# Kernel tuning notes

Hardware: AMD Instinct MI355X
Metric: run time of the kernel (lower is better)

Reference implementation:

```python
import jax, jax.numpy as jnp
import numpy as np

EPS = 1e-5
PROJ_EPS = 1e-5
MAX_TANH_ARG = 15.0
NUM_LAYERS = 2

def _norm(x):
    return jnp.sqrt(jnp.sum(x * x, axis=-1, keepdims=True))

def log_map_zero(y):
    # Poincare ball log map at the origin: arctanh(||y||) * y / ||y||
    n = _norm(y)
    n_c = jnp.clip(n, EPS, 1.0 - PROJ_EPS)
    return jnp.arctanh(n_c) * y / jnp.maximum(n, EPS)

def exp_map_zero(v):
    # Poincare ball exp map at the origin: tanh(||v||) * v / ||v||
    n = _norm(v)
    n_c = jnp.clip(n, EPS, MAX_TANH_ARG)
    return jnp.tanh(n_c) * v / jnp.maximum(n, EPS)

def setup_inputs() -> dict:
    key = jax.random.key(0)
    k1, k2, k3, k4 = jax.random.split(key, 4)
    N, K, D = 50000, 32, 128
    # scale initial features so they lie inside the unit ball
    node_repr = jax.random.normal(k1, (N, D), dtype=jnp.float32) * 0.01
    adj_mat = jax.random.randint(k2, (N, K), 0, N, dtype=jnp.int32)
    weight = jax.random.uniform(k3, (N, K), dtype=jnp.float32)
    mask = jnp.ones((N, 1), dtype=jnp.float32)
    # learned params: one [D, D] matrix per layer (tie_weight=False, poincare)
    msg_weights = jax.random.normal(k4, (NUM_LAYERS, D, D), dtype=jnp.float32) * (1.0 / np.sqrt(D))
    return {"node_repr": node_repr, "adj_mat": adj_mat, "weight": weight,
            "mask": mask, "msg_weights": msg_weights}

def reference(node_repr, adj_mat, weight, mask, msg_weights):
    x = node_repr
    for step in range(NUM_LAYERS):
        # log map back to tangent space at origin (identity on first layer)
        x = (log_map_zero(x) if step > 0 else x) * mask
        msg = (x @ msg_weights[step]) * mask            # [N, D] dense projection
        nbr = msg[adj_mat]                              # [N, K, D] gather by adjacency
        combined = jnp.einsum('nk,nkd->nd', weight, nbr) * mask  # weighted neighbor sum (dropout p=0)
        x = exp_map_zero(combined) * mask               # back to the manifold
        x = jax.nn.relu(x) * mask                       # poincare activation
    return x
```

## Files before the change

### kernel.cpp

```cpp
#include <hip/hip_runtime.h>

#define EPS 1e-5f
#define PROJ_EPS 1e-5f
#define MAX_TANH_ARG 15.0f

typedef __bf16 bf16x8 __attribute__((ext_vector_type(8)));
typedef float f32x4 __attribute__((ext_vector_type(4)));

__device__ __forceinline__ unsigned short f2bf(float f) {
  unsigned u = __builtin_bit_cast(unsigned, f);
  u += 0x7fffu + ((u >> 16) & 1u);
  return (unsigned short)(u >> 16);
}
__device__ __forceinline__ float bf2f(unsigned short h) {
  return __builtin_bit_cast(float, ((unsigned)h) << 16);
}

union BF8 {
  unsigned short u[8];
  bf16x8 v;
  uint4 q;
};

__global__ void pack_w_kernel(const float* __restrict__ W,
                              unsigned short* __restrict__ wpack) {
  int tid = blockIdx.x * blockDim.x + threadIdx.x;
  if (tid >= 2 * 8 * 4 * 64) return;
  int lane = tid & 63;
  int s = (tid >> 6) & 3;
  int t = (tid >> 8) & 7;
  int layer = tid >> 11;
  int quad = lane >> 4;
  int n = t * 16 + (lane & 15);
  unsigned short* dst = wpack + ((size_t)((layer * 32 + t * 4 + s) * 64 + lane)) * 8;
  const float* src = W + (size_t)layer * 16384;
#pragma unroll
  for (int j = 0; j < 8; ++j) {
    int k = s * 32 + quad * 8 + j;
    dst[j] = f2bf(src[(size_t)k * 128 + n]);
  }
}

template <int MODE>
__global__ __launch_bounds__(256) void gemm_kernel(
    const float* __restrict__ xf, const unsigned short* __restrict__ xb,
    const float* __restrict__ scale_in, const unsigned short* __restrict__ wpack,
    unsigned short* __restrict__ msg, int N) {
  const int lane = threadIdx.x & 63;
  const int wv = threadIdx.x >> 6;
  const int m = lane & 15;
  const int quad = lane >> 4;
  const int base = blockIdx.x * 64 + wv * 16;
  const int row = base + m;
  const int rowc = row < N ? row : N - 1;
  const float scale = (row < N) ? scale_in[rowc] : 0.0f;

  f32x4 acc[8];
#pragma unroll
  for (int t = 0; t < 8; ++t) acc[t] = (f32x4){0.f, 0.f, 0.f, 0.f};

#pragma unroll
  for (int sk = 0; sk < 4; ++sk) {
    const int k0 = sk * 32 + quad * 8;
    BF8 a;
    if (MODE == 0) {
      const float4* xp = (const float4*)(xf + (size_t)rowc * 128 + k0);
      float4 p0 = xp[0], p1 = xp[1];
      a.u[0] = f2bf(p0.x * scale); a.u[1] = f2bf(p0.y * scale);
      a.u[2] = f2bf(p0.z * scale); a.u[3] = f2bf(p0.w * scale);
      a.u[4] = f2bf(p1.x * scale); a.u[5] = f2bf(p1.y * scale);
      a.u[6] = f2bf(p1.z * scale); a.u[7] = f2bf(p1.w * scale);
    } else {
      BF8 r;
      r.q = *(const uint4*)(xb + (size_t)rowc * 128 + k0);
#pragma unroll
      for (int j = 0; j < 8; ++j) a.u[j] = f2bf(bf2f(r.u[j]) * scale);
    }
#pragma unroll
    for (int t = 0; t < 8; ++t) {
      BF8 b;
      b.q = *(const uint4*)(wpack + (size_t)((t * 4 + sk) * 64 + lane) * 8);
      acc[t] = __builtin_amdgcn_mfma_f32_16x16x32_bf16(a.v, b.v, acc[t], 0, 0, 0);
    }
  }

#pragma unroll
  for (int t = 0; t < 8; ++t) {
    const int c = t * 16 + m;
#pragma unroll
    for (int r = 0; r < 4; ++r) {
      const int rr = base + quad * 4 + r;
      if (rr < N) msg[(size_t)rr * 128 + c] = f2bf(acc[t][r]);
    }
  }
}

template <int MODE>
__global__ __launch_bounds__(256) void gather_kernel(
    const unsigned short* __restrict__ msg, const int* __restrict__ adj,
    const float* __restrict__ wgt, unsigned short* __restrict__ x1out,
    float* __restrict__ lsout, float* __restrict__ out, int N) {
  const int lane = threadIdx.x & 63;
  const int gw = (int)((blockIdx.x * blockDim.x + threadIdx.x) >> 6);
  const int nw = (int)((gridDim.x * blockDim.x) >> 6);
  for (int n = gw; n < N; n += nw) {
    int idxv = 0;
    float wv = 0.f;
    if (lane < 32) {
      idxv = adj[(size_t)n * 32 + lane];
      wv = wgt[(size_t)n * 32 + lane];
    }
    float a0 = 0.f, a1 = 0.f;
#pragma unroll
    for (int k = 0; k < 32; ++k) {
      const int id = __shfl(idxv, k);
      const float wk = __shfl(wv, k);
      const unsigned pr = *(const unsigned*)(msg + (size_t)id * 128 + 2 * lane);
      a0 = fmaf(wk, bf2f((unsigned short)(pr & 0xffffu)), a0);
      a1 = fmaf(wk, bf2f((unsigned short)(pr >> 16)), a1);
    }
    float s2 = a0 * a0 + a1 * a1;
#pragma unroll
    for (int o = 32; o > 0; o >>= 1) s2 += __shfl_xor(s2, o);
    const float nrm = sqrtf(s2);
    const float ncl = fminf(fmaxf(nrm, EPS), MAX_TANH_ARG);
    const float esc = tanhf(ncl) / fmaxf(nrm, EPS);
    const float v0 = fmaxf(esc * a0, 0.f);
    const float v1 = fmaxf(esc * a1, 0.f);
    if (MODE == 0) {
      const unsigned pk = (unsigned)f2bf(v0) | ((unsigned)f2bf(v1) << 16);
      *(unsigned*)(x1out + (size_t)n * 128 + 2 * lane) = pk;
      float r2 = v0 * v0 + v1 * v1;
#pragma unroll
      for (int o = 32; o > 0; o >>= 1) r2 += __shfl_xor(r2, o);
      const float nr = sqrtf(r2);
      const float nc2 = fminf(fmaxf(nr, EPS), 1.0f - PROJ_EPS);
      const float ls = 0.5f * logf((1.0f + nc2) / (1.0f - nc2)) / fmaxf(nr, EPS);
      if (lane == 0) lsout[n] = ls;
    } else {
      *(float2*)(out + (size_t)n * 128 + 2 * lane) = make_float2(v0, v1);
    }
  }
}

extern "C" void kernel_launch(void* const* d_in, const int* in_sizes, int n_in,
                              void* d_out, int out_size, void* d_ws, size_t ws_size,
                              hipStream_t stream) {
  const float* node = (const float*)d_in[0];
  const int* adj = (const int*)d_in[1];
  const float* wgt = (const float*)d_in[2];
  const float* mask = (const float*)d_in[3];
  const float* mw = (const float*)d_in[4];
  float* out = (float*)d_out;
  const int N = in_sizes[0] / 128;

  char* ws = (char*)d_ws;
  unsigned short* wpack = (unsigned short*)ws;
  float* ls = (float*)(ws + 65536);
  size_t ls_bytes = ((size_t)N * 4 + 255) & ~(size_t)255;
  unsigned short* msg = (unsigned short*)(ws + 65536 + ls_bytes);
  unsigned short* x1 = (unsigned short*)d_out;

  hipLaunchKernelGGL(pack_w_kernel, dim3(16), dim3(256), 0, stream, mw, wpack);
  const int gb = (N + 63) / 64;
  hipLaunchKernelGGL((gemm_kernel<0>), dim3(gb), dim3(256), 0, stream,
                     node, (const unsigned short*)nullptr, mask, wpack, msg, N);
  hipLaunchKernelGGL((gather_kernel<0>), dim3(1024), dim3(256), 0, stream,
                     msg, adj, wgt, x1, ls, (float*)nullptr, N);
  hipLaunchKernelGGL((gemm_kernel<1>), dim3(gb), dim3(256), 0, stream,
                     (const float*)nullptr, x1, ls, wpack + 16384, msg, N);
  hipLaunchKernelGGL((gather_kernel<1>), dim3(1024), dim3(256), 0, stream,
                     msg, adj, wgt, (unsigned short*)nullptr, (float*)nullptr, out, N);
}
```

Baseline: 210.3 us.

## Stage GEMM output through LDS, apply row scale post-MFMA, pair nodes per wave in gather

The GEMM now applies the per-row scale after accumulation instead of rescaling inputs, stages the bf16 output tile in shared memory, and writes it back with coalesced 16-byte stores. The gather kernel handles two nodes per wave, using readlane for scalar index/weight broadcast so each iteration issues two independent gathers, and the grid is doubled. Mask handling is moved into the gather epilogue. This targets scattered narrow global stores and gather latency, at the cost of an LDS barrier and more registers.

```diff
diff --git a/kernel.cpp b/kernel.cpp
--- a/kernel.cpp
+++ b/kernel.cpp
@@ -6,6 +6,7 @@
 
 typedef __bf16 bf16x8 __attribute__((ext_vector_type(8)));
 typedef float f32x4 __attribute__((ext_vector_type(4)));
+typedef float f32x2 __attribute__((ext_vector_type(2)));
 
 __device__ __forceinline__ unsigned short f2bf(float f) {
   unsigned u = __builtin_bit_cast(unsigned, f);
@@ -44,16 +45,17 @@
 template <int MODE>
 __global__ __launch_bounds__(256) void gemm_kernel(
     const float* __restrict__ xf, const unsigned short* __restrict__ xb,
-    const float* __restrict__ scale_in, const unsigned short* __restrict__ wpack,
+    const float* __restrict__ rowscale, const unsigned short* __restrict__ wpack,
     unsigned short* __restrict__ msg, int N) {
+  __shared__ unsigned short tile[64][136];
   const int lane = threadIdx.x & 63;
   const int wv = threadIdx.x >> 6;
   const int m = lane & 15;
   const int quad = lane >> 4;
-  const int base = blockIdx.x * 64 + wv * 16;
-  const int row = base + m;
+  const int base = blockIdx.x * 64;
+  const int wbase = base + wv * 16;
+  const int row = wbase + m;
   const int rowc = row < N ? row : N - 1;
-  const float scale = (row < N) ? scale_in[rowc] : 0.0f;
 
   f32x4 acc[8];
 #pragma unroll
@@ -66,15 +68,12 @@
     if (MODE == 0) {
       const float4* xp = (const float4*)(xf + (size_t)rowc * 128 + k0);
       float4 p0 = xp[0], p1 = xp[1];
-      a.u[0] = f2bf(p0.x * scale); a.u[1] = f2bf(p0.y * scale);
-      a.u[2] = f2bf(p0.z * scale); a.u[3] = f2bf(p0.w * scale);
-      a.u[4] = f2bf(p1.x * scale); a.u[5] = f2bf(p1.y * scale);
-      a.u[6] = f2bf(p1.z * scale); a.u[7] = f2bf(p1.w * scale);
+      a.u[0] = f2bf(p0.x); a.u[1] = f2bf(p0.y);
+      a.u[2] = f2bf(p0.z); a.u[3] = f2bf(p0.w);
+      a.u[4] = f2bf(p1.x); a.u[5] = f2bf(p1.y);
+      a.u[6] = f2bf(p1.z); a.u[7] = f2bf(p1.w);
     } else {
-      BF8 r;
-      r.q = *(const uint4*)(xb + (size_t)rowc * 128 + k0);
-#pragma unroll
-      for (int j = 0; j < 8; ++j) a.u[j] = f2bf(bf2f(r.u[j]) * scale);
+      a.q = *(const uint4*)(xb + (size_t)rowc * 128 + k0);
     }
 #pragma unroll
     for (int t = 0; t < 8; ++t) {
@@ -84,13 +83,33 @@
     }
   }
 
+  float sc[4];
+#pragma unroll
+  for (int r = 0; r < 4; ++r) {
+    int rr = wbase + quad * 4 + r;
+    rr = rr < N ? rr : N - 1;
+    float s = rowscale[rr];
+    sc[r] = (MODE == 0) ? s * s : s;
+  }
 #pragma unroll
   for (int t = 0; t < 8; ++t) {
     const int c = t * 16 + m;
 #pragma unroll
     for (int r = 0; r < 4; ++r) {
-      const int rr = base + quad * 4 + r;
-      if (rr < N) msg[(size_t)rr * 128 + c] = f2bf(acc[t][r]);
+      tile[wv * 16 + quad * 4 + r][c] = f2bf(acc[t][r] * sc[r]);
+    }
+  }
+  __syncthreads();
+
+#pragma unroll
+  for (int i = 0; i < 4; ++i) {
+    const int flat = i * 4096 + (int)threadIdx.x * 16;
+    const int r64 = flat >> 8;
+    const int colb = flat & 255;
+    const int grow = base + r64;
+    if (grow < N) {
+      *(uint4*)((char*)msg + (size_t)grow * 256 + colb) =
+          *(const uint4*)&tile[r64][colb >> 1];
     }
   }
 }
@@ -98,47 +117,74 @@
 template <int MODE>
 __global__ __launch_bounds__(256) void gather_kernel(
     const unsigned short* __restrict__ msg, const int* __restrict__ adj,
-    const float* __restrict__ wgt, unsigned short* __restrict__ x1out,
-    float* __restrict__ lsout, float* __restrict__ out, int N) {
+    const float* __restrict__ wgt, const float* __restrict__ mask,
+    unsigned short* __restrict__ x1out, float* __restrict__ lsout,
+    float* __restrict__ out, int N) {
   const int lane = threadIdx.x & 63;
+  const int half = lane >> 5;
+  const int j = lane & 31;
   const int gw = (int)((blockIdx.x * blockDim.x + threadIdx.x) >> 6);
   const int nw = (int)((gridDim.x * blockDim.x) >> 6);
-  for (int n = gw; n < N; n += nw) {
+  const int npairs = (N + 1) >> 1;
+
+  for (int p = gw; p < npairs; p += nw) {
+    const int nA = p * 2;
+    const int nB = nA + 1;
+    const int myn = nA + half;
     int idxv = 0;
     float wv = 0.f;
-    if (lane < 32) {
-      idxv = adj[(size_t)n * 32 + lane];
-      wv = wgt[(size_t)n * 32 + lane];
-    }
-    float a0 = 0.f, a1 = 0.f;
+    if (myn < N) {
+      idxv = adj[(size_t)myn * 32 + j];
+      wv = wgt[(size_t)myn * 32 + j];
+    }
+    f32x2 aA = {0.f, 0.f}, aB = {0.f, 0.f};
 #pragma unroll
     for (int k = 0; k < 32; ++k) {
-      const int id = __shfl(idxv, k);
-      const float wk = __shfl(wv, k);
-      const unsigned pr = *(const unsigned*)(msg + (size_t)id * 128 + 2 * lane);
-      a0 = fmaf(wk, bf2f((unsigned short)(pr & 0xffffu)), a0);
-      a1 = fmaf(wk, bf2f((unsigned short)(pr >> 16)), a1);
-    }
-    float s2 = a0 * a0 + a1 * a1;
-#pragma unroll
-    for (int o = 32; o > 0; o >>= 1) s2 += __shfl_xor(s2, o);
-    const float nrm = sqrtf(s2);
-    const float ncl = fminf(fmaxf(nrm, EPS), MAX_TANH_ARG);
-    const float esc = tanhf(ncl) / fmaxf(nrm, EPS);
-    const float v0 = fmaxf(esc * a0, 0.f);
-    const float v1 = fmaxf(esc * a1, 0.f);
-    if (MODE == 0) {
-      const unsigned pk = (unsigned)f2bf(v0) | ((unsigned)f2bf(v1) << 16);
-      *(unsigned*)(x1out + (size_t)n * 128 + 2 * lane) = pk;
-      float r2 = v0 * v0 + v1 * v1;
-#pragma unroll
-      for (int o = 32; o > 0; o >>= 1) r2 += __shfl_xor(r2, o);
-      const float nr = sqrtf(r2);
-      const float nc2 = fminf(fmaxf(nr, EPS), 1.0f - PROJ_EPS);
-      const float ls = 0.5f * logf((1.0f + nc2) / (1.0f - nc2)) / fmaxf(nr, EPS);
-      if (lane == 0) lsout[n] = ls;
-    } else {
-      *(float2*)(out + (size_t)n * 128 + 2 * lane) = make_float2(v0, v1);
+      const int idA = __builtin_amdgcn_readlane(idxv, k);
+      const float wA = __builtin_bit_cast(
+          float, __builtin_amdgcn_readlane(__builtin_bit_cast(int, wv), k));
+      const int idB = __builtin_amdgcn_readlane(idxv, 32 + k);
+      const float wB = __builtin_bit_cast(
+          float, __builtin_amdgcn_readlane(__builtin_bit_cast(int, wv), 32 + k));
+      const unsigned prA = *(const unsigned*)(msg + (size_t)idA * 128 + 2 * lane);
+      const unsigned prB = *(const unsigned*)(msg + (size_t)idB * 128 + 2 * lane);
+      f32x2 mA, mB;
+      mA.x = __builtin_bit_cast(float, prA << 16);
+      mA.y = __builtin_bit_cast(float, prA & 0xffff0000u);
+      mB.x = __builtin_bit_cast(float, prB << 16);
+      mB.y = __builtin_bit_cast(float, prB & 0xffff0000u);
+      aA = __builtin_elementwise_fma(mA, (f32x2){wA, wA}, aA);
+      aB = __builtin_elementwise_fma(mB, (f32x2){wB, wB}, aB);
+    }
+
+#pragma unroll
+    for (int which = 0; which < 2; ++which) {
+      const int n = which ? nB : nA;
+      if (n >= N) continue;
+      const f32x2 a = which ? aB : aA;
+      const float mm = mask[n];
+      const float c0 = a.x * mm, c1 = a.y * mm;
+      float s2 = c0 * c0 + c1 * c1;
+#pragma unroll
+      for (int o = 32; o > 0; o >>= 1) s2 += __shfl_xor(s2, o);
+      const float nrm = sqrtf(s2);
+      const float ncl = fminf(fmaxf(nrm, EPS), MAX_TANH_ARG);
+      const float esc = tanhf(ncl) / fmaxf(nrm, EPS) * mm;
+      const float v0 = fmaxf(esc * c0, 0.f) * mm;
+      const float v1 = fmaxf(esc * c1, 0.f) * mm;
+      if (MODE == 0) {
+        const unsigned pk = (unsigned)f2bf(v0) | ((unsigned)f2bf(v1) << 16);
+        *(unsigned*)(x1out + (size_t)n * 128 + 2 * lane) = pk;
+        float r2 = v0 * v0 + v1 * v1;
+#pragma unroll
+        for (int o = 32; o > 0; o >>= 1) r2 += __shfl_xor(r2, o);
+        const float nr = sqrtf(r2);
+        const float nc2 = fminf(fmaxf(nr, EPS), 1.0f - PROJ_EPS);
+        const float ls = 0.5f * logf((1.0f + nc2) / (1.0f - nc2)) / fmaxf(nr, EPS);
+        if (lane == 0) lsout[n] = ls * mm * mm;
+      } else {
+        *(float2*)(out + (size_t)n * 128 + 2 * lane) = make_float2(v0, v1);
+      }
     }
   }
 }
@@ -156,7 +202,7 @@
 
   char* ws = (char*)d_ws;
   unsigned short* wpack = (unsigned short*)ws;
-  float* ls = (float*)(ws + 65536);
+  float* lsp = (float*)(ws + 65536);
   size_t ls_bytes = ((size_t)N * 4 + 255) & ~(size_t)255;
   unsigned short* msg = (unsigned short*)(ws + 65536 + ls_bytes);
   unsigned short* x1 = (unsigned short*)d_out;
@@ -165,10 +211,10 @@
   const int gb = (N + 63) / 64;
   hipLaunchKernelGGL((gemm_kernel<0>), dim3(gb), dim3(256), 0, stream,
                      node, (const unsigned short*)nullptr, mask, wpack, msg, N);
-  hipLaunchKernelGGL((gather_kernel<0>), dim3(1024), dim3(256), 0, stream,
-                     msg, adj, wgt, x1, ls, (float*)nullptr, N);
+  hipLaunchKernelGGL((gather_kernel<0>), dim3(2048), dim3(256), 0, stream,
+                     msg, adj, wgt, mask, x1, lsp, (float*)nullptr, N);
   hipLaunchKernelGGL((gemm_kernel<1>), dim3(gb), dim3(256), 0, stream,
-                     (const float*)nullptr, x1, ls, wpack + 16384, msg, N);
-  hipLaunchKernelGGL((gather_kernel<1>), dim3(1024), dim3(256), 0, stream,
-                     msg, adj, wgt, (unsigned short*)nullptr, (float*)nullptr, out, N);
-}
+                     (const float*)nullptr, x1, lsp, wpack + 16384, msg, N);
+  hipLaunchKernelGGL((gather_kernel<1>), dim3(2048), dim3(256), 0, stream,
+                     msg, adj, wgt, mask, (unsigned short*)nullptr, (float*)nullptr, out, N);
+}
```

Result: slower. 216.8 us (+3.1%).
